# Optimization experiments

Hardware: AMD Instinct MI355X
Metric: run time of the kernel (lower is better)

Reference implementation:

```python
import jax, jax.numpy as jnp
import numpy as np

B, S, D, H, TM = 4, 512, 512, 8, 20
DH = D // H
LAMBDA_REG = 1e-3


def setup_inputs() -> dict:
    key = jax.random.key(0)
    ks = jax.random.split(key, 12)

    def lin(k, o, i):
        return (jax.random.normal(k, (o, i), jnp.float32) / np.float32(np.sqrt(i)))

    return {
        "x": jax.random.normal(ks[0], (B, S, D), jnp.float32),
        "Wq": lin(ks[1], D, D), "Wk": lin(ks[2], D, D), "Wv": lin(ks[3], D, D),
        "Wo": lin(ks[4], D, D), "bo": jnp.zeros((D,), jnp.float32),
        "gw1": lin(ks[5], 64, D), "gb1": jnp.zeros((64,), jnp.float32),
        "gw2": lin(ks[6], 32, 64), "gb2": jnp.zeros((32,), jnp.float32),
        "gw3": lin(ks[7], 1, 32), "gb3": jnp.zeros((1,), jnp.float32),
        "cw1": lin(ks[8], 32, D), "cb1": jnp.zeros((32,), jnp.float32),
        "cw2": lin(ks[9], 1, 32), "cb2": jnp.zeros((1,), jnp.float32),
        "alpha": jnp.float32(np.exp(-1.0 / 5.0)),   # tau_syn = 5
        "beta": jnp.float32(np.exp(-1.0 / 20.0)),   # tau_mem = 20
    }


def reference(x, Wq, Wk, Wv, Wo, bo, gw1, gb1, gw2, gb2, gw3, gb3,
              cw1, cb1, cw2, cb2, alpha, beta):
    scale = jnp.float32(DH ** -0.5)

    # adaptive window sizes T_i in [1, TM]
    g = jax.nn.sigmoid(jax.nn.relu(jax.nn.relu(x @ gw1.T + gb1) @ gw2.T + gb2) @ gw3.T + gb3)
    c = jax.nn.sigmoid(jax.nn.relu(x @ cw1.T + cb1) @ cw2.T + cb2)
    combined = (0.7 * g + 0.3 * c)[..., 0]                       # [B,S]
    T_i = jnp.clip(jnp.ceil(combined * TM), 1, TM).astype(jnp.int32)
    mask = (jnp.arange(TM)[None, None, :] < T_i[:, :, None]).astype(x.dtype)  # [B,S,TM]

    def lif_spikes(inp):  # inp [B,S,D] -> spikes [B,S,TM,D] (zeroed past T_i)
        def step(carry, _):
            v, i = carry
            i = alpha * i + inp
            v = beta * v + i
            s = jnp.where(v >= 1.0, 1.0, 0.0).astype(inp.dtype)
            v = v * (1.0 - s)  # v_reset = 0
            return (v, i), s
        z = jnp.zeros_like(inp)
        _, sp = jax.lax.scan(step, (z, z), None, length=TM)      # [TM,B,S,D]
        return jnp.moveaxis(sp, 0, 2) * mask[..., None]

    q_sp = lif_spikes(x @ Wq.T).reshape(B, S, TM, H, DH)
    k_sp = lif_spikes(x @ Wk.T).reshape(B, S, TM, H, DH)
    v_sp = lif_spikes(x @ Wv.T).reshape(B, S, TM, H, DH)

    scores = jnp.einsum('bithd,bjthd->bhij', q_sp, k_sp) * scale
    attn = jax.nn.softmax(scores, axis=-1)                       # dropout is eval-mode identity
    v_mean = v_sp.mean(axis=2).transpose(0, 2, 1, 3)             # [B,H,S,DH]
    out = jnp.einsum('bhij,bhjd->bhid', attn, v_mean)
    out = out.transpose(0, 2, 1, 3).reshape(B, S, D) @ Wo.T + bo
    reg = jnp.float32(LAMBDA_REG) * T_i.astype(x.dtype).mean()
    return out, attn, reg, T_i
```

## Files before the change

kernel.cpp:

```cpp
#include <hip/hip_runtime.h>
#include <cstdint>


typedef __attribute__((ext_vector_type(8))) _Float16 f16x8;
typedef __attribute__((ext_vector_type(4))) float f32x4;

__device__ __forceinline__ float sep_mad(float a, float b, float c) {
    float t = a * b;
    asm volatile("" : "+v"(t));
    return t + c;
}

union HU4 { _Float16 h[4]; ushort4 u; };
union HU8 { _Float16 h[8]; uint4 u; };
union HU2 { _Float16 h[2]; unsigned u; };

__device__ __forceinline__ void split4(float4 v, HU4& hi, HU4& lo) {
    hi.h[0] = (_Float16)v.x; lo.h[0] = (_Float16)(v.x - (float)hi.h[0]);
    hi.h[1] = (_Float16)v.y; lo.h[1] = (_Float16)(v.y - (float)hi.h[1]);
    hi.h[2] = (_Float16)v.z; lo.h[2] = (_Float16)(v.z - (float)hi.h[2]);
    hi.h[3] = (_Float16)v.w; lo.h[3] = (_Float16)(v.w - (float)hi.h[3]);
}

__device__ __forceinline__ void cast4(float4 v, HU4& hi) {
    hi.h[0] = (_Float16)v.x; hi.h[1] = (_Float16)v.y;
    hi.h[2] = (_Float16)v.z; hi.h[3] = (_Float16)v.w;
}

__global__ __launch_bounds__(256) void k_gemm3(
    const float* __restrict__ X,
    const float* __restrict__ Wq, const float* __restrict__ Wk,
    const float* __restrict__ Wv, const float* __restrict__ gw1,
    const float* __restrict__ cw1,
    float* __restrict__ Y)
{
    __shared__ _Float16 AsH[4][64][8];
    __shared__ _Float16 BsH[4][64][8];
    __shared__ _Float16 AsL[4][64][8];
    __shared__ _Float16 BsL[4][64][8];

    const int bn = blockIdx.x * 64, bm = blockIdx.y * 64;
    const int tid = threadIdx.x, w = tid >> 6, l = tid & 63;
    const int mB = (w & 1) * 32, nB = (w >> 1) * 32;
    const int sr = tid >> 2, sk = tid & 3;
    const int fr = l & 15, fk = l >> 4;
    const bool gate = (bn >= 1536);

    const float* asrc = X + (bm + sr) * 512;
    const int brow = bn + sr;
    const float* bsrc;
    bool bvalid = true;
    if      (brow < 512)  bsrc = Wq  + brow * 512;
    else if (brow < 1024) bsrc = Wk  + (brow - 512) * 512;
    else if (brow < 1536) bsrc = Wv  + (brow - 1024) * 512;
    else if (brow < 1600) bsrc = gw1 + (brow - 1536) * 512;
    else if (brow < 1632) bsrc = cw1 + (brow - 1600) * 512;
    else { bsrc = Wq; bvalid = false; }

    f32x4 acc[2][2] = {};
    const float4 z4{0.f, 0.f, 0.f, 0.f};

    float4 pa0 = *(const float4*)(asrc + sk * 8);
    float4 pa1 = *(const float4*)(asrc + sk * 8 + 4);
    float4 pb0 = bvalid ? *(const float4*)(bsrc + sk * 8)     : z4;
    float4 pb1 = bvalid ? *(const float4*)(bsrc + sk * 8 + 4) : z4;

    for (int k0 = 0; k0 < 512; k0 += 32) {
        __syncthreads();
        if (gate) {
            HU4 h0, l0, h1, l1;
            split4(pa0, h0, l0); split4(pa1, h1, l1);
            *(ushort4*)&AsH[sk][sr][0] = h0.u; *(ushort4*)&AsH[sk][sr][4] = h1.u;
            *(ushort4*)&AsL[sk][sr][0] = l0.u; *(ushort4*)&AsL[sk][sr][4] = l1.u;
            split4(pb0, h0, l0); split4(pb1, h1, l1);
            *(ushort4*)&BsH[sk][sr][0] = h0.u; *(ushort4*)&BsH[sk][sr][4] = h1.u;
            *(ushort4*)&BsL[sk][sr][0] = l0.u; *(ushort4*)&BsL[sk][sr][4] = l1.u;
        } else {
            HU4 h0, h1;
            cast4(pa0, h0); cast4(pa1, h1);
            *(ushort4*)&AsH[sk][sr][0] = h0.u; *(ushort4*)&AsH[sk][sr][4] = h1.u;
            cast4(pb0, h0); cast4(pb1, h1);
            *(ushort4*)&BsH[sk][sr][0] = h0.u; *(ushort4*)&BsH[sk][sr][4] = h1.u;
        }
        __syncthreads();
        const int kn = (k0 + 32) & 511;
        pa0 = *(const float4*)(asrc + kn + sk * 8);
        pa1 = *(const float4*)(asrc + kn + sk * 8 + 4);
        if (bvalid) {
            pb0 = *(const float4*)(bsrc + kn + sk * 8);
            pb1 = *(const float4*)(bsrc + kn + sk * 8 + 4);
        }

        f16x8 ah[2];
#pragma unroll
        for (int mt = 0; mt < 2; mt++)
            ah[mt] = *(const f16x8*)&AsH[fk][mB + mt * 16 + fr][0];
        if (gate) {
            f16x8 al[2];
#pragma unroll
            for (int mt = 0; mt < 2; mt++)
                al[mt] = *(const f16x8*)&AsL[fk][mB + mt * 16 + fr][0];
#pragma unroll
            for (int nt = 0; nt < 2; nt++) {
                f16x8 bh = *(const f16x8*)&BsH[fk][nB + nt * 16 + fr][0];
                f16x8 bl = *(const f16x8*)&BsL[fk][nB + nt * 16 + fr][0];
#pragma unroll
                for (int mt = 0; mt < 2; mt++) {
                    acc[mt][nt] = __builtin_amdgcn_mfma_f32_16x16x32_f16(ah[mt], bh, acc[mt][nt], 0, 0, 0);
                    acc[mt][nt] = __builtin_amdgcn_mfma_f32_16x16x32_f16(ah[mt], bl, acc[mt][nt], 0, 0, 0);
                    acc[mt][nt] = __builtin_amdgcn_mfma_f32_16x16x32_f16(al[mt], bh, acc[mt][nt], 0, 0, 0);
                }
            }
        } else {
#pragma unroll
            for (int nt = 0; nt < 2; nt++) {
                f16x8 bh = *(const f16x8*)&BsH[fk][nB + nt * 16 + fr][0];
#pragma unroll
                for (int mt = 0; mt < 2; mt++)
                    acc[mt][nt] = __builtin_amdgcn_mfma_f32_16x16x32_f16(ah[mt], bh, acc[mt][nt], 0, 0, 0);
            }
        }
    }

#pragma unroll
    for (int mt = 0; mt < 2; mt++) {
#pragma unroll
        for (int nt = 0; nt < 2; nt++) {
            const int j = bn + nB + nt * 16 + fr;
#pragma unroll
            for (int rr = 0; rr < 4; rr++) {
                const int i = bm + mB + mt * 16 + fk * 4 + rr;
                Y[i * 1664 + j] = acc[mt][nt][rr];
            }
        }
    }
}

__global__ __launch_bounds__(256) void k_lif(
    const float* __restrict__ qkvh1,
    const float* __restrict__ gb1, const float* __restrict__ cb1,
    const float* __restrict__ gw2, const float* __restrict__ gb2,
    const float* __restrict__ gw3, const float* __restrict__ gb3,
    const float* __restrict__ cw2, const float* __restrict__ cb2,
    const float* __restrict__ pAlpha, const float* __restrict__ pBeta,
    unsigned long long* __restrict__ qbits,
    unsigned long long* __restrict__ kbits,
    _Float16* __restrict__ vmT,
    int* __restrict__ Ti, float* __restrict__ ti_out)
{
    __shared__ _Float16 cnts[64][10];
    __shared__ float h1s[8][100];
    __shared__ float w2s[32][65];
    __shared__ float h2s[8][36];
    __shared__ int tis[8];
    const int tid = threadIdx.x;
    const int wid = tid >> 6, lane = tid & 63;
    const int bh = blockIdx.y, s0 = blockIdx.x * 8;
    const int b = bh >> 3, h = bh & 7;
    const float alpha = pAlpha[0], beta = pBeta[0];

    for (int i = tid; i < 2048; i += 256) w2s[i >> 6][i & 63] = gw2[i];
    for (int i = tid; i < 768; i += 256) {
        const int r = i / 96, c = i % 96;
        const float v = qkvh1[(long)(b * 512 + s0 + r) * 1664 + 1536 + c]
                        + (c < 64 ? gb1[c] : cb1[c - 64]);
        h1s[r][c] = fmaxf(v, 0.f);
    }
    __syncthreads();
    {
        const int tok = tid >> 5, o2 = tid & 31;
        float a = gb2[o2];
        for (int k = 0; k < 64; k++) a = fmaf(w2s[o2][k], h1s[tok][k], a);
        h2s[tok][o2] = fmaxf(a, 0.f);
    }
    __syncthreads();
    if (tid < 8) {
        const int tok = tid;
        float gg = gb3[0], cc = cb2[0];
        for (int k = 0; k < 32; k++) {
            gg = fmaf(gw3[k], h2s[tok][k], gg);
            cc = fmaf(cw2[k], h1s[tok][64 + k], cc);
        }
        float g = 1.f / (1.f + expf(-gg));
        float c = 1.f / (1.f + expf(-cc));
        float p1 = 0.7f * g, p2 = 0.3f * c;
        asm volatile("" : "+v"(p1), "+v"(p2));
        float comb = p1 + p2;
        float tf = ceilf(comb * 20.0f);
        tf = fminf(fmaxf(tf, 1.f), 20.f);
        tis[tok] = (int)tf;
        Ti[b * 512 + s0 + tok] = (int)tf;
        ti_out[b * 512 + s0 + tok] = tf;
    }
    __syncthreads();

    const float* qrow0 = qkvh1 + (long)(b * 512 + s0 + wid) * 1664 + h * 64 + lane;
    float cq = qrow0[0], ck = qrow0[512], cv = qrow0[1024];

    for (int r = 0; r < 2; r++) {
        const int tl = r * 4 + wid;
        const int s = s0 + tl;
        float nq = 0.f, nk = 0.f, nv = 0.f;
        if (r < 1) {
            const float* qr = qkvh1 + (long)(b * 512 + s + 4) * 1664 + h * 64 + lane;
            nq = qr[0]; nk = qr[512]; nv = qr[1024];
        }
        const int T = tis[tl];
        float iq = 0.f, vq = 0.f, ik = 0.f, vk = 0.f, iv = 0.f, vv = 0.f;
        int cnt = 0;
        const int base = (bh * 20) * 512 + s;
#pragma unroll
        for (int t = 0; t < 20; t++) {
            iq = sep_mad(alpha, iq, cq); vq = sep_mad(beta, vq, iq);
            bool sq = vq >= 1.0f; vq = sq ? 0.f : vq;
            ik = sep_mad(alpha, ik, ck); vk = sep_mad(beta, vk, ik);
            bool sk = vk >= 1.0f; vk = sk ? 0.f : vk;
            iv = sep_mad(alpha, iv, cv); vv = sep_mad(beta, vv, iv);
            bool sv = vv >= 1.0f; vv = sv ? 0.f : vv;
            bool act = t < T;
            unsigned long long mq = __ballot(sq && act);
            unsigned long long mk = __ballot(sk && act);
            if (lane == 0) {
                qbits[base + t * 512] = mq;
                kbits[base + t * 512] = mk;
            }
            cnt += (sv && act) ? 1 : 0;
        }
        cnts[lane][tl] = (_Float16)((float)cnt / 20.0f);
        cq = nq; ck = nk; cv = nv;
    }
    __syncthreads();
    const int d = tid >> 2, q = tid & 3;
    HU2 o;
    o.h[0] = cnts[d][q * 2];
    o.h[1] = cnts[d][q * 2 + 1];
    *(unsigned*)(vmT + (bh * 64 + d) * 512 + s0 + q * 2) = o.u;
}

__global__ __launch_bounds__(256) void k_scores_av(
    const unsigned long long* __restrict__ qbits,
    const unsigned long long* __restrict__ kbits,
    float* __restrict__ attn,
    const int* __restrict__ Ti, float* __restrict__ regp,
    const _Float16* __restrict__ vmT,
    _Float16* __restrict__ hout)
{
    const int bh = blockIdx.x >> 5;
    const int i0 = (blockIdx.x & 31) * 16;
    const int base = bh * 20 * 512;
    __shared__ unsigned long long qs[20][16];
    __shared__ _Float16 sc16[16][520];
    const int tid = threadIdx.x;
    for (int idx = tid; idx < 320; idx += 256) {
        int t = idx >> 4, r = idx & 15;
        qs[t][r] = qbits[base + t * 512 + i0 + r];
    }
    int Tmax = 0;
    const int tb = (bh >> 3) * 512 + i0;
#pragma unroll
    for (int r = 0; r < 16; r++) Tmax = max(Tmax, Ti[tb + r]);
    __syncthreads();

    {
        const unsigned long long* kbp = kbits + base + 2 * tid;
        int acc0[16] = {}, acc1[16] = {};
        for (int tc = 0; tc < 4; tc++) {
            if (tc * 5 >= Tmax) break;
            unsigned long long kv0[5], kv1[5];
#pragma unroll
            for (int t = 0; t < 5; t++) {
                ulonglong2 kk = *(const ulonglong2*)(kbp + (tc * 5 + t) * 512);
                kv0[t] = kk.x; kv1[t] = kk.y;
            }
#pragma unroll
            for (int r = 0; r < 16; r++) {
#pragma unroll
                for (int t = 0; t < 5; t++) {
                    unsigned long long qv = qs[tc * 5 + t][r];
                    acc0[r] += __popcll(qv & kv0[t]);
                    acc1[r] += __popcll(qv & kv1[t]);
                }
            }
        }
#pragma unroll
        for (int r = 0; r < 16; r++) {
            HU2 p;
            p.h[0] = (_Float16)((float)acc0[r] * 0.125f);
            p.h[1] = (_Float16)((float)acc1[r] * 0.125f);
            *(unsigned*)&sc16[r][2 * tid] = p.u;
        }
    }
    __syncthreads();

    const int wid = tid >> 6, lane = tid & 63;
#pragma unroll
    for (int rr = 0; rr < 4; rr++) {
        const int r = wid * 4 + rr;
        float vals[8];
        float m = -1e30f;
#pragma unroll
        for (int k = 0; k < 8; k++) { vals[k] = (float)sc16[r][lane + 64 * k]; m = fmaxf(m, vals[k]); }
#pragma unroll
        for (int off = 32; off; off >>= 1) m = fmaxf(m, __shfl_xor(m, off));
        float sum = 0.f;
#pragma unroll
        for (int k = 0; k < 8; k++) { vals[k] = expf(vals[k] - m); sum += vals[k]; }
#pragma unroll
        for (int off = 32; off; off >>= 1) sum += __shfl_xor(sum, off);
        float* arow = attn + ((long)bh * 512 + (i0 + r)) * 512;
#pragma unroll
        for (int k = 0; k < 8; k++) {
            const float o = vals[k] / sum;
            arow[lane + 64 * k] = o;
            sc16[r][lane + 64 * k] = (_Float16)o;
        }
    }

    if (blockIdx.x == 0 && tid < 64) {
        int s = 0;
        for (int k = tid; k < 2048; k += 64) s += Ti[k];
#pragma unroll
        for (int off = 32; off; off >>= 1) s += __shfl_xor(s, off);
        if (tid == 0) regp[0] = 1e-3f * ((float)s / 2048.0f);
    }
    __syncthreads();

    const int fr = lane & 15, fk = lane >> 4;
    const int b = bh >> 3, h = bh & 7;
    f32x4 acc = {};
    const _Float16* bsrc = vmT + (bh * 64 + wid * 16 + fr) * 512;
#pragma unroll
    for (int k0 = 0; k0 < 512; k0 += 32) {
        f16x8 av = *(const f16x8*)&sc16[fr][k0 + fk * 8];
        f16x8 bv = *(const f16x8*)(bsrc + k0 + fk * 8);
        acc = __builtin_amdgcn_mfma_f32_16x16x32_f16(av, bv, acc, 0, 0, 0);
    }
    const int d = wid * 16 + fr;
#pragma unroll
    for (int rr = 0; rr < 4; rr++) {
        const int i = i0 + fk * 4 + rr;
        hout[(b * 512 + i) * 512 + h * 64 + d] = (_Float16)acc[rr];
    }
}

__global__ __launch_bounds__(256) void k_gemmWo(
    const _Float16* __restrict__ A, const float* __restrict__ Wo,
    const float* __restrict__ bias, float* __restrict__ Y)
{
    __shared__ _Float16 As[4][32][8];
    __shared__ _Float16 Bs[4][64][8];

    const int bn = blockIdx.x * 64, bm = blockIdx.y * 32;
    const int tid = threadIdx.x, w = tid >> 6, l = tid & 63;
    const int nB = w * 16;
    const int sr = tid >> 2, sk = tid & 3;
    const int ar = tid >> 3, ak = tid & 3;
    const int fr = l & 15, fk = l >> 4;

    f32x4 acc[2] = {};

    const float* bsrc = Wo + (bn + sr) * 512;
    const bool doA = ((tid & 4) == 0);
    uint4 pA = {};
    if (doA) pA = *(const uint4*)(A + (bm + ar) * 512 + ak * 8);
    float4 pb0 = *(const float4*)(bsrc + sk * 8);
    float4 pb1 = *(const float4*)(bsrc + sk * 8 + 4);

    for (int k0 = 0; k0 < 512; k0 += 32) {
        __syncthreads();
        {
            HU4 h0, h1;
            cast4(pb0, h0); cast4(pb1, h1);
            if (doA) *(uint4*)&As[ak][ar][0] = pA;
            *(ushort4*)&Bs[sk][sr][0] = h0.u; *(ushort4*)&Bs[sk][sr][4] = h1.u;
        }
        __syncthreads();
        const int kn = (k0 + 32) & 511;
        if (doA) pA = *(const uint4*)(A + (bm + ar) * 512 + kn + ak * 8);
        pb0 = *(const float4*)(bsrc + kn + sk * 8);
        pb1 = *(const float4*)(bsrc + kn + sk * 8 + 4);

        f16x8 bh = *(const f16x8*)&Bs[fk][nB + fr][0];
#pragma unroll
        for (int mt = 0; mt < 2; mt++) {
            f16x8 ah = *(const f16x8*)&As[fk][mt * 16 + fr][0];
            acc[mt] = __builtin_amdgcn_mfma_f32_16x16x32_f16(ah, bh, acc[mt], 0, 0, 0);
        }
    }

#pragma unroll
    for (int mt = 0; mt < 2; mt++) {
        const int j = bn + nB + fr;
        const float badd = bias[j];
#pragma unroll
        for (int rr = 0; rr < 4; rr++) {
            const int i = bm + mt * 16 + fk * 4 + rr;
            Y[i * 512 + j] = acc[mt][rr] + badd;
        }
    }
}

extern "C" void kernel_launch(void* const* d_in, const int* in_sizes, int n_in,
                              void* d_out, int out_size, void* d_ws, size_t ws_size,
                              hipStream_t stream)
{
    const float* x    = (const float*)d_in[0];
    const float* Wq   = (const float*)d_in[1];
    const float* Wk   = (const float*)d_in[2];
    const float* Wv   = (const float*)d_in[3];
    const float* Wo   = (const float*)d_in[4];
    const float* bo   = (const float*)d_in[5];
    const float* gw1  = (const float*)d_in[6];
    const float* gb1  = (const float*)d_in[7];
    const float* gw2  = (const float*)d_in[8];
    const float* gb2  = (const float*)d_in[9];
    const float* gw3  = (const float*)d_in[10];
    const float* gb3  = (const float*)d_in[11];
    const float* cw1  = (const float*)d_in[12];
    const float* cb1  = (const float*)d_in[13];
    const float* cw2  = (const float*)d_in[14];
    const float* cb2  = (const float*)d_in[15];
    const float* alpha = (const float*)d_in[16];
    const float* beta  = (const float*)d_in[17];

    float* out   = (float*)d_out;
    float* attn  = out + 1048576;
    float* regp  = out + 1048576 + 8388608;
    float* tiout = regp + 1;

    char* ws = (char*)d_ws;
    float*    qkvh1  = (float*)ws;
    unsigned long long* qb = (unsigned long long*)(ws + 13631488);
    unsigned long long* kb = (unsigned long long*)(ws + 16252928);
    _Float16* vmT    = (_Float16*)(ws + 18874368);
    _Float16* hout_h = (_Float16*)(ws + 20971520);
    int*      Ti     = (int*)(ws + 23068672);

    k_gemm3<<<dim3(26, 32), 256, 0, stream>>>(x, Wq, Wk, Wv, gw1, cw1, qkvh1);
    k_lif<<<dim3(64, 32), 256, 0, stream>>>(qkvh1, gb1, cb1, gw2, gb2, gw3, gb3,
                                            cw2, cb2, alpha, beta, qb, kb, vmT, Ti, tiout);
    k_scores_av<<<1024, 256, 0, stream>>>(qb, kb, attn, Ti, regp, vmT, hout_h);
    k_gemmWo<<<dim3(8, 64), 256, 0, stream>>>(hout_h, Wo, bo, out);
}
```

Before: 94.17 us.

## Fuse LIF spike generation into QKV GEMM epilogue and defer T_i masking

The LIF recurrence now runs in the QKV GEMM epilogue, reading the tile staged in shared memory, so the 13 MB fp32 QKV intermediate is never written or read back. Q/K spikes are emitted unmasked as ballot bitmasks and V spikes as per-element 20-bit words. A small gating kernel computes T_i separately. The scores/AV kernel applies the T_i mask on the fly and rebuilds v_mean by popcount. This cuts global traffic and one pass, but the AV loop now does strided 4-byte gathers of vbits per MFMA operand, which may be uncoalesced.

```diff
diff --git a/kernel.cpp b/kernel.cpp
--- a/kernel.cpp
+++ b/kernel.cpp
@@ -32,12 +32,17 @@
     const float* __restrict__ Wq, const float* __restrict__ Wk,
     const float* __restrict__ Wv, const float* __restrict__ gw1,
     const float* __restrict__ cw1,
-    float* __restrict__ Y)
+    const float* __restrict__ pAlpha, const float* __restrict__ pBeta,
+    unsigned long long* __restrict__ qbits,
+    unsigned long long* __restrict__ kbits,
+    unsigned* __restrict__ vbits,
+    float* __restrict__ h1buf)
 {
     __shared__ _Float16 AsH[4][64][8];
     __shared__ _Float16 BsH[4][64][8];
-    __shared__ _Float16 AsL[4][64][8];
-    __shared__ _Float16 BsL[4][64][8];
+    __shared__ float LT[64][64];
+    _Float16 (*AsL)[64][8] = reinterpret_cast<_Float16 (*)[64][8]>(&LT[0][0]);
+    _Float16 (*BsL)[64][8] = reinterpret_cast<_Float16 (*)[64][8]>(((char*)&LT[0][0]) + 4096);
 
     const int bn = blockIdx.x * 64, bm = blockIdx.y * 64;
     const int tid = threadIdx.x, w = tid >> 6, l = tid & 63;
@@ -122,59 +127,95 @@
         }
     }
 
-#pragma unroll
-    for (int mt = 0; mt < 2; mt++) {
-#pragma unroll
-        for (int nt = 0; nt < 2; nt++) {
-            const int j = bn + nB + nt * 16 + fr;
-#pragma unroll
-            for (int rr = 0; rr < 4; rr++) {
-                const int i = bm + mB + mt * 16 + fk * 4 + rr;
-                Y[i * 1664 + j] = acc[mt][nt][rr];
-            }
-        }
-    }
-}
-
-__global__ __launch_bounds__(256) void k_lif(
-    const float* __restrict__ qkvh1,
+    if (gate) {
+#pragma unroll
+        for (int mt = 0; mt < 2; mt++) {
+#pragma unroll
+            for (int nt = 0; nt < 2; nt++) {
+                const int jc = (bn - 1536) + nB + nt * 16 + fr;
+#pragma unroll
+                for (int rr = 0; rr < 4; rr++) {
+                    const int i = bm + mB + mt * 16 + fk * 4 + rr;
+                    h1buf[i * 128 + jc] = acc[mt][nt][rr];
+                }
+            }
+        }
+        return;
+    }
+
+#pragma unroll
+    for (int mt = 0; mt < 2; mt++)
+#pragma unroll
+        for (int nt = 0; nt < 2; nt++)
+#pragma unroll
+            for (int rr = 0; rr < 4; rr++)
+                LT[mB + mt * 16 + fk * 4 + rr][nB + nt * 16 + fr] = acc[mt][nt][rr];
+    __syncthreads();
+
+    const int p = bn >> 9;
+    const int h = (bn & 511) >> 6;
+    const float alpha = pAlpha[0], beta = pBeta[0];
+    for (int tt = 0; tt < 16; tt++) {
+        const int tok = w * 16 + tt;
+        const int gtok = bm + tok;
+        const int b = gtok >> 9, s = gtok & 511;
+        const float inp = LT[tok][l];
+        float ii = 0.f, vv = 0.f;
+        if (p < 2) {
+            unsigned long long* dst = (p == 0) ? qbits : kbits;
+            const long base = ((long)((b * 8 + h) * 20)) * 512 + s;
+#pragma unroll
+            for (int t = 0; t < 20; t++) {
+                ii = sep_mad(alpha, ii, inp); vv = sep_mad(beta, vv, ii);
+                bool sp = vv >= 1.0f; vv = sp ? 0.f : vv;
+                unsigned long long m = __ballot(sp);
+                if (l == 0) dst[base + t * 512] = m;
+            }
+        } else {
+            unsigned vw = 0;
+#pragma unroll
+            for (int t = 0; t < 20; t++) {
+                ii = sep_mad(alpha, ii, inp); vv = sep_mad(beta, vv, ii);
+                bool sp = vv >= 1.0f; vv = sp ? 0.f : vv;
+                vw |= ((unsigned)sp) << t;
+            }
+            vbits[(long)(b * 512 + s) * 512 + h * 64 + l] = vw;
+        }
+    }
+}
+
+__global__ __launch_bounds__(256) void k_gates2(
+    const float* __restrict__ h1raw,
     const float* __restrict__ gb1, const float* __restrict__ cb1,
     const float* __restrict__ gw2, const float* __restrict__ gb2,
     const float* __restrict__ gw3, const float* __restrict__ gb3,
     const float* __restrict__ cw2, const float* __restrict__ cb2,
-    const float* __restrict__ pAlpha, const float* __restrict__ pBeta,
-    unsigned long long* __restrict__ qbits,
-    unsigned long long* __restrict__ kbits,
-    _Float16* __restrict__ vmT,
     int* __restrict__ Ti, float* __restrict__ ti_out)
 {
-    __shared__ _Float16 cnts[64][10];
-    __shared__ float h1s[8][100];
+    __shared__ float h1s[32][100];
     __shared__ float w2s[32][65];
-    __shared__ float h2s[8][36];
-    __shared__ int tis[8];
+    __shared__ float h2s[32][36];
+    const int tok0 = blockIdx.x * 32;
     const int tid = threadIdx.x;
-    const int wid = tid >> 6, lane = tid & 63;
-    const int bh = blockIdx.y, s0 = blockIdx.x * 8;
-    const int b = bh >> 3, h = bh & 7;
-    const float alpha = pAlpha[0], beta = pBeta[0];
 
     for (int i = tid; i < 2048; i += 256) w2s[i >> 6][i & 63] = gw2[i];
-    for (int i = tid; i < 768; i += 256) {
+    for (int i = tid; i < 3072; i += 256) {
         const int r = i / 96, c = i % 96;
-        const float v = qkvh1[(long)(b * 512 + s0 + r) * 1664 + 1536 + c]
-                        + (c < 64 ? gb1[c] : cb1[c - 64]);
+        const float v = h1raw[(long)(tok0 + r) * 128 + c] + (c < 64 ? gb1[c] : cb1[c - 64]);
         h1s[r][c] = fmaxf(v, 0.f);
     }
     __syncthreads();
-    {
-        const int tok = tid >> 5, o2 = tid & 31;
+
+#pragma unroll
+    for (int it = 0; it < 4; it++) {
+        const int tok = (tid >> 5) + it * 8, o2 = tid & 31;
         float a = gb2[o2];
         for (int k = 0; k < 64; k++) a = fmaf(w2s[o2][k], h1s[tok][k], a);
         h2s[tok][o2] = fmaxf(a, 0.f);
     }
     __syncthreads();
-    if (tid < 8) {
+
+    if (tid < 32) {
         const int tok = tid;
         float gg = gb3[0], cc = cb2[0];
         for (int k = 0; k < 32; k++) {
@@ -188,81 +229,48 @@
         float comb = p1 + p2;
         float tf = ceilf(comb * 20.0f);
         tf = fminf(fmaxf(tf, 1.f), 20.f);
-        tis[tok] = (int)tf;
-        Ti[b * 512 + s0 + tok] = (int)tf;
-        ti_out[b * 512 + s0 + tok] = tf;
-    }
-    __syncthreads();
-
-    const float* qrow0 = qkvh1 + (long)(b * 512 + s0 + wid) * 1664 + h * 64 + lane;
-    float cq = qrow0[0], ck = qrow0[512], cv = qrow0[1024];
-
-    for (int r = 0; r < 2; r++) {
-        const int tl = r * 4 + wid;
-        const int s = s0 + tl;
-        float nq = 0.f, nk = 0.f, nv = 0.f;
-        if (r < 1) {
-            const float* qr = qkvh1 + (long)(b * 512 + s + 4) * 1664 + h * 64 + lane;
-            nq = qr[0]; nk = qr[512]; nv = qr[1024];
-        }
-        const int T = tis[tl];
-        float iq = 0.f, vq = 0.f, ik = 0.f, vk = 0.f, iv = 0.f, vv = 0.f;
-        int cnt = 0;
-        const int base = (bh * 20) * 512 + s;
-#pragma unroll
-        for (int t = 0; t < 20; t++) {
-            iq = sep_mad(alpha, iq, cq); vq = sep_mad(beta, vq, iq);
-            bool sq = vq >= 1.0f; vq = sq ? 0.f : vq;
-            ik = sep_mad(alpha, ik, ck); vk = sep_mad(beta, vk, ik);
-            bool sk = vk >= 1.0f; vk = sk ? 0.f : vk;
-            iv = sep_mad(alpha, iv, cv); vv = sep_mad(beta, vv, iv);
-            bool sv = vv >= 1.0f; vv = sv ? 0.f : vv;
-            bool act = t < T;
-            unsigned long long mq = __ballot(sq && act);
-            unsigned long long mk = __ballot(sk && act);
-            if (lane == 0) {
-                qbits[base + t * 512] = mq;
-                kbits[base + t * 512] = mk;
-            }
-            cnt += (sv && act) ? 1 : 0;
-        }
-        cnts[lane][tl] = (_Float16)((float)cnt / 20.0f);
-        cq = nq; ck = nk; cv = nv;
-    }
-    __syncthreads();
-    const int d = tid >> 2, q = tid & 3;
-    HU2 o;
-    o.h[0] = cnts[d][q * 2];
-    o.h[1] = cnts[d][q * 2 + 1];
-    *(unsigned*)(vmT + (bh * 64 + d) * 512 + s0 + q * 2) = o.u;
+        Ti[tok0 + tok] = (int)tf;
+        ti_out[tok0 + tok] = tf;
+    }
 }
 
 __global__ __launch_bounds__(256) void k_scores_av(
     const unsigned long long* __restrict__ qbits,
     const unsigned long long* __restrict__ kbits,
+    const unsigned* __restrict__ vbits,
     float* __restrict__ attn,
     const int* __restrict__ Ti, float* __restrict__ regp,
-    const _Float16* __restrict__ vmT,
     _Float16* __restrict__ hout)
 {
     const int bh = blockIdx.x >> 5;
     const int i0 = (blockIdx.x & 31) * 16;
     const int base = bh * 20 * 512;
+    const int b = bh >> 3, h = bh & 7;
     __shared__ unsigned long long qs[20][16];
     __shared__ _Float16 sc16[16][520];
+    __shared__ unsigned tmask[512];
     const int tid = threadIdx.x;
+
+    for (int i = tid; i < 512; i += 256) {
+        const int T = Ti[b * 512 + i];
+        tmask[i] = (1u << T) - 1u;
+    }
+    __syncthreads();
+
+    int Tmax = 0;
+    const int tb = b * 512 + i0;
+#pragma unroll
+    for (int r = 0; r < 16; r++) Tmax = max(Tmax, Ti[tb + r]);
     for (int idx = tid; idx < 320; idx += 256) {
         int t = idx >> 4, r = idx & 15;
-        qs[t][r] = qbits[base + t * 512 + i0 + r];
-    }
-    int Tmax = 0;
-    const int tb = (bh >> 3) * 512 + i0;
-#pragma unroll
-    for (int r = 0; r < 16; r++) Tmax = max(Tmax, Ti[tb + r]);
+        unsigned long long w = qbits[base + t * 512 + i0 + r];
+        qs[t][r] = ((tmask[i0 + r] >> t) & 1u) ? w : 0ull;
+    }
     __syncthreads();
 
     {
         const unsigned long long* kbp = kbits + base + 2 * tid;
+        const unsigned m0 = tmask[2 * tid], m1 = tmask[2 * tid + 1];
         int acc0[16] = {}, acc1[16] = {};
         for (int tc = 0; tc < 4; tc++) {
             if (tc * 5 >= Tmax) break;
@@ -270,7 +278,8 @@
 #pragma unroll
             for (int t = 0; t < 5; t++) {
                 ulonglong2 kk = *(const ulonglong2*)(kbp + (tc * 5 + t) * 512);
-                kv0[t] = kk.x; kv1[t] = kk.y;
+                kv0[t] = ((m0 >> (tc * 5 + t)) & 1u) ? kk.x : 0ull;
+                kv1[t] = ((m1 >> (tc * 5 + t)) & 1u) ? kk.y : 0ull;
             }
 #pragma unroll
             for (int r = 0; r < 16; r++) {
@@ -326,13 +335,18 @@
     __syncthreads();
 
     const int fr = lane & 15, fk = lane >> 4;
-    const int b = bh >> 3, h = bh & 7;
     f32x4 acc = {};
-    const _Float16* bsrc = vmT + (bh * 64 + wid * 16 + fr) * 512;
+    const unsigned* vb = vbits + (long)b * 512 * 512 + h * 64 + wid * 16 + fr;
 #pragma unroll
     for (int k0 = 0; k0 < 512; k0 += 32) {
         f16x8 av = *(const f16x8*)&sc16[fr][k0 + fk * 8];
-        f16x8 bv = *(const f16x8*)(bsrc + k0 + fk * 8);
+        f16x8 bv;
+#pragma unroll
+        for (int e = 0; e < 8; e++) {
+            const int s = k0 + fk * 8 + e;
+            const unsigned vw = vb[(long)s * 512];
+            bv[e] = (_Float16)((float)__popc(vw & tmask[s]) / 20.0f);
+        }
         acc = __builtin_amdgcn_mfma_f32_16x16x32_f16(av, bv, acc, 0, 0, 0);
     }
     const int d = wid * 16 + fr;
@@ -429,16 +443,17 @@
     float* tiout = regp + 1;
 
     char* ws = (char*)d_ws;
-    float*    qkvh1  = (float*)ws;
-    unsigned long long* qb = (unsigned long long*)(ws + 13631488);
-    unsigned long long* kb = (unsigned long long*)(ws + 16252928);
-    _Float16* vmT    = (_Float16*)(ws + 18874368);
-    _Float16* hout_h = (_Float16*)(ws + 20971520);
-    int*      Ti     = (int*)(ws + 23068672);
-
-    k_gemm3<<<dim3(26, 32), 256, 0, stream>>>(x, Wq, Wk, Wv, gw1, cw1, qkvh1);
-    k_lif<<<dim3(64, 32), 256, 0, stream>>>(qkvh1, gb1, cb1, gw2, gb2, gw3, gb3,
-                                            cw2, cb2, alpha, beta, qb, kb, vmT, Ti, tiout);
-    k_scores_av<<<1024, 256, 0, stream>>>(qb, kb, attn, Ti, regp, vmT, hout_h);
+    unsigned long long* qb = (unsigned long long*)ws;
+    unsigned long long* kb = (unsigned long long*)(ws + 2621440);
+    unsigned* vbits  = (unsigned*)(ws + 5242880);
+    float*    h1buf  = (float*)(ws + 9437184);
+    _Float16* hout_h = (_Float16*)(ws + 10485760);
+    int*      Ti     = (int*)(ws + 12582912);
+
+    k_gemm3<<<dim3(26, 32), 256, 0, stream>>>(x, Wq, Wk, Wv, gw1, cw1,
+                                              alpha, beta, qb, kb, vbits, h1buf);
+    k_gates2<<<64, 256, 0, stream>>>(h1buf, gb1, cb1, gw2, gb2, gw3, gb3,
+                                     cw2, cb2, Ti, tiout);
+    k_scores_av<<<1024, 256, 0, stream>>>(qb, kb, vbits, attn, Ti, regp, hout_h);
     k_gemmWo<<<dim3(8, 64), 256, 0, stream>>>(hout_h, Wo, bo, out);
 }
```

Result: slower. 119.6 us (+27.0%).
